# Kernel optimization log

Measured on AMD Instinct MI355X. Metric: run time of the kernel, lower is better.

The kernel has to match this reference:

```python
import jax, jax.numpy as jnp
import numpy as np

D = 1024       # d_model
H = 16         # n_heads
N = 8          # ortho_dim
NSKEW = N * (N - 1) // 2
MAX_ANGLE = 0.5
B, T = 4, 4096
IDX_I, IDX_J = np.triu_indices(N, k=1)


def setup_inputs() -> dict:
    key = jax.random.key(0)
    ks = jax.random.split(key, 8)
    s = 0.02
    w = lambda k, shape: jax.random.normal(k, shape, jnp.float32) * s
    return {
        "x": jax.random.normal(ks[0], (B, T, D), jnp.float32),
        "W_skew": w(ks[1], (D, H * NSKEW)),
        "W_k": w(ks[2], (D, H * N)),
        "W_v": w(ks[3], (D, H * N)),
        "W_q": w(ks[4], (D, H * N)),
        "W_beta": w(ks[5], (D, H)),
        "b_beta": w(ks[6], (H,)),
        "W_o": w(ks[7], (H * N, D)),
    }


def _forward(x, W_skew, W_k, W_v, W_q, W_beta, b_beta, W_o):
    Bb, Tt, _ = x.shape
    # skew-symmetric generator -> rotation O_t = expm(skew)
    skew_flat = MAX_ANGLE * jnp.tanh(x @ W_skew).reshape(Bb, Tt, H, NSKEW)
    skew = jnp.zeros((Bb, Tt, H, N, N), x.dtype)
    skew = skew.at[..., IDX_I, IDX_J].set(skew_flat)
    skew = skew.at[..., IDX_J, IDX_I].set(-skew_flat)
    O = jax.vmap(jax.scipy.linalg.expm)(skew.reshape(-1, N, N)).reshape(Bb, Tt, H, N, N)

    k = (x @ W_k).reshape(Bb, Tt, H, N)
    k = k / jnp.maximum(jnp.linalg.norm(k, axis=-1, keepdims=True), 1e-6)
    v = (x @ W_v).reshape(Bb, Tt, H, N)
    q = (x @ W_q).reshape(Bb, Tt, H, N)
    beta = jax.nn.sigmoid(x @ W_beta + b_beta)  # [B,T,H]

    def step(c, inp):
        O_t, k_t, v_t, b_t, q_t = inp  # [B,H,n,n], [B,H,n], ...
        # rotation conjugation: O c O^T
        c_rot = jnp.einsum('bhij,bhjk,bhlk->bhil', O_t, c, O_t)
        # rank-1 erase: c_rot - beta * k (k^T c_rot); rank-1 write: + beta * k v^T
        kc = jnp.einsum('bhi,bhij->bhj', k_t, c_rot)
        b = b_t[..., None, None]
        c_new = c_rot - b * k_t[..., None] * kc[..., None, :] + b * k_t[..., None] * v_t[..., None, :]
        o_t = jnp.einsum('bhi,bhij->bhj', q_t, c_new)  # readout q . c_t
        return c_new, o_t

    c0 = jnp.zeros((Bb, H, N, N), x.dtype)
    tfirst = lambda a: jnp.moveaxis(a, 1, 0)
    _, o = jax.lax.scan(step, c0, (tfirst(O), tfirst(k), tfirst(v), tfirst(beta), tfirst(q)))
    o = jnp.moveaxis(o, 0, 1).reshape(Bb, Tt, H * N)
    return o @ W_o


def reference(x, W_skew, W_k, W_v, W_q, W_beta, b_beta, W_o):
    return _forward(x, W_skew, W_k, W_v, W_q, W_beta, b_beta, W_o)
```

## Files before the change

kernel.cpp:

```cpp
#include <hip/hip_runtime.h>

typedef unsigned short u16;
typedef unsigned int u32;
typedef __attribute__((ext_vector_type(4))) float f32x4;
typedef __attribute__((ext_vector_type(8))) short short8;
typedef __attribute__((ext_vector_type(4))) unsigned int u32x4;

#define DEV __device__ __forceinline__

DEV float bf2f(u16 u){ union{u32 i; float f;} x; x.i = ((u32)u)<<16; return x.f; }
DEV u16 f2bf(float f){ union{u32 i; float f;} x; x.f = f; u32 r = x.i + 0x7fffu + ((x.i>>16)&1u); return (u16)(r>>16); }

union U8 { u16 u[8]; short8 s; };

DEV void gl16(const u16* g, u16* l){
  __builtin_amdgcn_global_load_lds(
      (const __attribute__((address_space(1))) u32*)g,
      (__attribute__((address_space(3))) u32*)l, 16, 0, 0);
}

DEV float fast_htanh(float v){
  float vc = fminf(fmaxf(v, -15.f), 15.f);
  float e = __expf(2.f*vc);
  return 0.5f*(e - 1.f)*__builtin_amdgcn_rcpf(e + 1.f);
}
DEV float fast_sigmoid(float v){
  float e = __expf(-v);
  return __builtin_amdgcn_rcpf(1.f + e);
}

__global__ __launch_bounds__(256) void splitx_kernel(const float* __restrict__ x,
    u16* __restrict__ xh, u16* __restrict__ xl)
{
  size_t base = ((size_t)blockIdx.x*256 + threadIdx.x) * 8;
  f32x4 a = *(const f32x4*)(x + base), b = *(const f32x4*)(x + base + 4);
  U8 h, l;
  #pragma unroll
  for (int e=0;e<4;e++){
    u16 hh = f2bf(a[e]); h.u[e]   = hh; l.u[e]   = f2bf(a[e] - bf2f(hh));
    u16 gg = f2bf(b[e]); h.u[4+e] = gg; l.u[4+e] = f2bf(b[e] - bf2f(gg));
  }
  *(short8*)(xh + base) = h.s;
  *(short8*)(xl + base) = l.s;
}

__global__ __launch_bounds__(256) void concat_kernel(
    const float* __restrict__ Wskew, const float* __restrict__ Wk, const float* __restrict__ Wv,
    const float* __restrict__ Wq, const float* __restrict__ Wbeta, const float* __restrict__ Wo,
    u16* __restrict__ Wh, u16* __restrict__ Wl, u16* __restrict__ WoT)
{
  int idx = blockIdx.x*256 + threadIdx.x;
  if (idx < 896*1024){
    int n = idx >> 10, kk = idx & 1023;
    float v;
    if (n < 448)      v = Wskew[kk*448 + n];
    else if (n < 576) v = Wk[kk*128 + (n-448)];
    else if (n < 704) v = Wv[kk*128 + (n-576)];
    else if (n < 832) v = Wq[kk*128 + (n-704)];
    else if (n < 848) v = Wbeta[kk*16 + (n-832)];
    else              v = 0.f;
    u16 h = f2bf(v);
    Wh[idx] = h;
    Wl[idx] = f2bf(v - bf2f(h));
  } else {
    int r = idx - 896*1024;
    int n = r >> 7, kk = r & 127;
    WoT[r] = f2bf(Wo[kk*1024 + n]);
  }
}

__global__ __launch_bounds__(256) void gemm_proj_kernel(
    const u16* __restrict__ Ah, const u16* __restrict__ Al,
    const u16* __restrict__ Bh, const u16* __restrict__ Bl,
    float* __restrict__ C, const float* __restrict__ bias)
{
  __shared__ u16 L[2*4*4096];
  const int tid = threadIdx.x;
  const int wave = tid >> 6;
  const int lane = tid & 63;
  const int quad = lane >> 4, l15 = lane & 15;
  const int m0 = blockIdx.x * 128, n0 = blockIdx.y * 128;
  const bool full = (blockIdx.y < 4);
  const int wm = (wave >> 1) * 64, wn = (wave & 1) * 64;
  const bool wantLow = full && !(blockIdx.y == 3 && wn == 64);
  const bool skipBl1 = (blockIdx.y == 3);
  const int K = 1024, ldc = 896;
  const int sr = tid >> 2;
  const int sc = tid & 3;
  const int fS = (sr & 3) ^ ((sr >> 2) & 3);
  const int scS = ((sc ^ fS) << 3);
  const size_t gA0 = (size_t)(m0 + sr)*K + scS, gA1 = gA0 + (size_t)64*K;
  const size_t gB0 = (size_t)(n0 + sr)*K + scS, gB1 = gB0 + (size_t)64*K;
  const int d0 = tid*8, d1 = d0 + 2048;
  const int fR = (l15 & 3) ^ ((l15 >> 2) & 3);
  const int rq = ((quad ^ fR) << 3);

  auto STAGE = [&](int buf, int kb){
    u16* Lb = L + buf*16384;
    gl16(Ah + gA0 + kb, Lb + d0);
    gl16(Ah + gA1 + kb, Lb + d1);
    gl16(Bh + gB0 + kb, Lb + 4096 + d0);
    gl16(Bh + gB1 + kb, Lb + 4096 + d1);
    if (full){
      gl16(Al + gA0 + kb, Lb + 8192 + d0);
      gl16(Al + gA1 + kb, Lb + 8192 + d1);
      gl16(Bl + gB0 + kb, Lb + 12288 + d0);
      if (!skipBl1) gl16(Bl + gB1 + kb, Lb + 12288 + d1);
    }
  };

  f32x4 acc[4][4] = {};
  STAGE(0, 0);
  __syncthreads();
  int cur = 0;
  for (int kb = 0; kb < K; kb += 32){
    if (kb + 32 < K) STAGE(cur^1, kb + 32);
    u16* Lb = L + cur*16384;
    short8 afh[4], bfh[4];
    #pragma unroll
    for (int mi=0;mi<4;mi++) afh[mi] = *(const short8*)&Lb[(wm + mi*16 + l15)*32 + rq];
    #pragma unroll
    for (int ni=0;ni<4;ni++) bfh[ni] = *(const short8*)&Lb[4096 + (wn + ni*16 + l15)*32 + rq];
    #pragma unroll
    for (int mi=0;mi<4;mi++)
      #pragma unroll
      for (int ni=0;ni<4;ni++)
        acc[mi][ni] = __builtin_amdgcn_mfma_f32_16x16x32_bf16(afh[mi], bfh[ni], acc[mi][ni], 0,0,0);
    if (wantLow){
      short8 afl[4], bfl[4];
      #pragma unroll
      for (int mi=0;mi<4;mi++) afl[mi] = *(const short8*)&Lb[8192 + (wm + mi*16 + l15)*32 + rq];
      #pragma unroll
      for (int ni=0;ni<4;ni++) bfl[ni] = *(const short8*)&Lb[12288 + (wn + ni*16 + l15)*32 + rq];
      #pragma unroll
      for (int mi=0;mi<4;mi++)
        #pragma unroll
        for (int ni=0;ni<4;ni++){
          acc[mi][ni] = __builtin_amdgcn_mfma_f32_16x16x32_bf16(afh[mi], bfl[ni], acc[mi][ni], 0,0,0);
          acc[mi][ni] = __builtin_amdgcn_mfma_f32_16x16x32_bf16(afl[mi], bfh[ni], acc[mi][ni], 0,0,0);
        }
    }
    __syncthreads();
    cur ^= 1;
  }
  #pragma unroll
  for (int mi=0;mi<4;mi++){
    #pragma unroll
    for (int ni=0;ni<4;ni++){
      const int col = n0 + wn + ni*16 + l15;
      const int rb_ = m0 + wm + mi*16 + quad*4;
      #pragma unroll
      for (int r=0;r<4;r++){
        float v = acc[mi][ni][r];
        const int row = rb_ + r;
        if (col < 448) v = fast_htanh(v);
        else if (col >= 832 && col < 848) v = fast_sigmoid(v + bias[col-832]);
        C[(size_t)row*ldc + col] = v;
      }
    }
  }
}

__global__ __launch_bounds__(256) void gemm_out_kernel(
    const u16* __restrict__ A, const u16* __restrict__ Bt, float* __restrict__ C)
{
  __shared__ u16 L[2*2*4096];
  const int tid = threadIdx.x;
  const int wave = tid >> 6;
  const int lane = tid & 63;
  const int quad = lane >> 4, l15 = lane & 15;
  const int m0 = blockIdx.x * 128, n0 = blockIdx.y * 128;
  const int wm = (wave >> 1) * 64, wn = (wave & 1) * 64;
  const int K = 128, ldc = 1024;
  const int sr = tid >> 2;
  const int sc = tid & 3;
  const int fS = (sr & 3) ^ ((sr >> 2) & 3);
  const int scS = ((sc ^ fS) << 3);
  const size_t gA0 = (size_t)(m0 + sr)*K + scS, gA1 = gA0 + (size_t)64*K;
  const size_t gB0 = (size_t)(n0 + sr)*K + scS, gB1 = gB0 + (size_t)64*K;
  const int d0 = tid*8, d1 = d0 + 2048;
  const int fR = (l15 & 3) ^ ((l15 >> 2) & 3);
  const int rq = ((quad ^ fR) << 3);

  auto STAGE = [&](int buf, int kb){
    u16* Lb = L + buf*8192;
    gl16(A  + gA0 + kb, Lb + d0);
    gl16(A  + gA1 + kb, Lb + d1);
    gl16(Bt + gB0 + kb, Lb + 4096 + d0);
    gl16(Bt + gB1 + kb, Lb + 4096 + d1);
  };

  f32x4 acc[4][4] = {};
  STAGE(0, 0);
  __syncthreads();
  int cur = 0;
  for (int kb = 0; kb < K; kb += 32){
    if (kb + 32 < K) STAGE(cur^1, kb + 32);
    u16* Lb = L + cur*8192;
    short8 af[4], bf8[4];
    #pragma unroll
    for (int mi=0;mi<4;mi++) af[mi] = *(const short8*)&Lb[(wm + mi*16 + l15)*32 + rq];
    #pragma unroll
    for (int ni=0;ni<4;ni++) bf8[ni] = *(const short8*)&Lb[4096 + (wn + ni*16 + l15)*32 + rq];
    #pragma unroll
    for (int mi=0;mi<4;mi++)
      #pragma unroll
      for (int ni=0;ni<4;ni++)
        acc[mi][ni] = __builtin_amdgcn_mfma_f32_16x16x32_bf16(af[mi], bf8[ni], acc[mi][ni], 0,0,0);
    __syncthreads();
    cur ^= 1;
  }
  #pragma unroll
  for (int mi=0;mi<4;mi++)
    #pragma unroll
    for (int ni=0;ni<4;ni++){
      const int col = n0 + wn + ni*16 + l15;
      const int rb_ = m0 + wm + mi*16 + quad*4;
      #pragma unroll
      for (int r=0;r<4;r++)
        C[(size_t)(rb_ + r)*ldc + col] = acc[mi][ni][r];
    }
}

__device__ constexpr int TRI_I[28] = {0,0,0,0,0,0,0, 1,1,1,1,1,1, 2,2,2,2,2, 3,3,3,3, 4,4,4, 5,5, 6};
__device__ constexpr int TRI_J[28] = {1,2,3,4,5,6,7, 2,3,4,5,6,7, 3,4,5,6,7, 4,5,6,7, 5,6,7, 6,7, 7};

__global__ __launch_bounds__(64) __attribute__((amdgpu_waves_per_eu(1, 2)))
void expm_scan_kernel(const float* __restrict__ proj, u16* __restrict__ ORbf, float* __restrict__ Pfin)
{
  __shared__ float S0[16*64*4];
  const int t = threadIdx.x;
  const int s = blockIdx.x >> 6, c = blockIdx.x & 63;
  const int b = s >> 4, h = s & 15;
  const int row = b*4096 + c*64 + t;
  const float* sk = proj + (size_t)row*896 + h*28;

  float v[28];
  {
    f32x4 vv[7];
    #pragma unroll
    for (int i=0;i<7;i++) vv[i] = *(const f32x4*)(sk + 4*i);
    #pragma unroll
    for (int i=0;i<28;i++) v[i] = vv[i>>2][i&3] * 0.0625f;
  }

  float M[64], T[64];
  #pragma unroll
  for (int i=0;i<8;i++){
    #pragma unroll
    for (int jj=0;jj<8;jj++){
      float bv = 0.f;
      if (i < jj){ const int k = i*7 - (i*(i-1))/2 + jj - i - 1; bv =  v[k]; }
      if (i > jj){ const int k = jj*7 - (jj*(jj-1))/2 + i - jj - 1; bv = -v[k]; }
      M[i*8+jj] = bv*(1.f/6.f) + ((i==jj)?1.f:0.f);
    }
  }
  const float coef[5] = {0.2f, 0.25f, 1.f/3.f, 0.5f, 1.f};
  #pragma unroll
  for (int st=0; st<5; st++){
    #pragma unroll
    for (int i=0;i<8;i++){
      float rowv[8];
      #pragma unroll
      for (int a=0;a<8;a++) rowv[a] = M[i*8+a];
      #pragma unroll
      for (int cc=0;cc<8;cc++){
        float acc = 0.f;
        #pragma unroll
        for (int a=0;a<8;a++){
          if (a == cc) continue;
          const int k = (a<cc) ? (a*7 - (a*(a-1))/2 + cc - a - 1)
                               : (cc*7 - (cc*(cc-1))/2 + a - cc - 1);
          if (a<cc) acc = fmaf( rowv[a], v[k], acc);
          else      acc = fmaf(-rowv[a], v[k], acc);
        }
        M[i*8+cc] = acc*coef[st] + ((i==cc)?1.f:0.f);
      }
    }
  }
  #pragma unroll
  for (int sq=0; sq<4; sq++){
    #pragma unroll
    for (int i=0;i<8;i++)
      #pragma unroll
      for (int cc=0;cc<8;cc++){
        float acc = 0.f;
        #pragma unroll
        for (int a=0;a<8;a++) acc = fmaf(M[i*8+a], M[a*8+cc], acc);
        T[i*8+cc] = acc;
      }
    #pragma unroll
    for (int f=0;f<64;f++) M[f] = T[f];
  }
  #pragma unroll
  for (int j=0;j<16;j++){
    f32x4 w = {M[4*j], M[4*j+1], M[4*j+2], M[4*j+3]};
    *(f32x4*)&S0[(j*64 + t)*4] = w;
  }
  __syncthreads();

  #pragma unroll
  for (int d=0; d<6; d++){
    const int off = 1 << d;
    if (t >= off){
      float Q[64];
      #pragma unroll
      for (int j=0;j<16;j++){
        f32x4 x = *(const f32x4*)&S0[(j*64 + (t-off))*4];
        Q[4*j]=x[0]; Q[4*j+1]=x[1]; Q[4*j+2]=x[2]; Q[4*j+3]=x[3];
      }
      #pragma unroll
      for (int i=0;i<8;i++){
        float r[8];
        #pragma unroll
        for (int cc=0;cc<8;cc++){
          float acc = 0.f;
          #pragma unroll
          for (int a=0;a<8;a++) acc = fmaf(M[i*8+a], Q[a*8+cc], acc);
          r[cc] = acc;
        }
        #pragma unroll
        for (int cc=0;cc<8;cc++) M[i*8+cc] = r[cc];
      }
    }
    if (d < 5){
      #pragma unroll
      for (int j=0;j<16;j++){
        f32x4 w = {M[4*j], M[4*j+1], M[4*j+2], M[4*j+3]};
        *(f32x4*)&S0[(j*64 + t)*4] = w;
      }
      __syncthreads();
    }
  }

  u16* dst = ORbf + ((size_t)s*4096 + (size_t)c*64 + t)*64;
  #pragma unroll
  for (int g=0; g<8; g++){
    u32 p0 = (u32)f2bf(M[0*8+g]) | ((u32)f2bf(M[1*8+g])<<16);
    u32 p1 = (u32)f2bf(M[2*8+g]) | ((u32)f2bf(M[3*8+g])<<16);
    u32 p2 = (u32)f2bf(M[4*8+g]) | ((u32)f2bf(M[5*8+g])<<16);
    u32 p3 = (u32)f2bf(M[6*8+g]) | ((u32)f2bf(M[7*8+g])<<16);
    u32x4 pk = {p0,p1,p2,p3};
    *(u32x4*)(void*)(dst + g*8) = pk;
  }
  if (t == 63){
    float* pf = Pfin + ((size_t)s*64 + c)*64;
    #pragma unroll
    for (int a=0;a<8;a++){
      f32x4 w  = {M[0*8+a], M[1*8+a], M[2*8+a], M[3*8+a]};
      f32x4 w2 = {M[4*8+a], M[5*8+a], M[6*8+a], M[7*8+a]};
      *(f32x4*)(pf + a*8)     = w;
      *(f32x4*)(pf + a*8 + 4) = w2;
    }
  }
}

DEV void load16(const float* p, f32x4* M){
  #pragma unroll
  for (int q=0;q<16;q++) M[q] = *(const f32x4*)(p + 4*q);
}
DEV void load16bf(const u16* p, f32x4* M){
  #pragma unroll
  for (int q=0;q<8;q++){
    u32x4 x = *(const u32x4*)(const void*)(p + q*8);
    f32x4 a = { bf2f((u16)x[0]), bf2f((u16)(x[0]>>16)), bf2f((u16)x[1]), bf2f((u16)(x[1]>>16)) };
    f32x4 b = { bf2f((u16)x[2]), bf2f((u16)(x[2]>>16)), bf2f((u16)x[3]), bf2f((u16)(x[3]>>16)) };
    M[2*q] = a; M[2*q+1] = b;
  }
}
DEV void rm_matvec8(const f32x4* M16, const float* x, float* res){
  #pragma unroll
  for (int i=0;i<8;i++){
    float acc = 0.f;
    #pragma unroll
    for (int a=0;a<8;a++) acc = fmaf(M16[2*i + (a>>2)][a&3], x[a], acc);
    res[i] = acc;
  }
}
DEV void cm_matvec8(const f32x4* M16, const float* x, float* res){
  #pragma unroll
  for (int i=0;i<8;i++){
    float acc = 0.f;
    #pragma unroll
    for (int a=0;a<8;a++) acc = fmaf(M16[2*a + (i>>2)][i&3], x[a], acc);
    res[i] = acc;
  }
}

__global__ __launch_bounds__(64) __attribute__((amdgpu_waves_per_eu(1, 2)))
void chunkscan_kernel(const float* __restrict__ Pfin, float* __restrict__ Rbase)
{
  __shared__ float S[64*68];
  const int t = threadIdx.x;
  const int s = blockIdx.x;
  float M[64];
  const float* qs = Pfin + ((size_t)s*64 + t)*64;
  #pragma unroll
  for (int j=0;j<16;j++){
    f32x4 x = *(const f32x4*)(qs + 4*j);
    M[4*j]=x[0]; M[4*j+1]=x[1]; M[4*j+2]=x[2]; M[4*j+3]=x[3];
  }
  #pragma unroll
  for (int j=0;j<16;j++){
    f32x4 w = {M[4*j],M[4*j+1],M[4*j+2],M[4*j+3]};
    *(f32x4*)&S[t*68 + 4*j] = w;
  }
  __syncthreads();
  #pragma unroll
  for (int d=0; d<6; d++){
    const int off = 1 << d;
    if (t >= off){
      float Q[64];
      const float* p = &S[(t-off)*68];
      #pragma unroll
      for (int j=0;j<16;j++){
        f32x4 x = *(const f32x4*)(p + 4*j);
        Q[4*j]=x[0]; Q[4*j+1]=x[1]; Q[4*j+2]=x[2]; Q[4*j+3]=x[3];
      }
      float R[64];
      #pragma unroll
      for (int cc=0;cc<8;cc++)
        #pragma unroll
        for (int i=0;i<8;i++){
          float acc = 0.f;
          #pragma unroll
          for (int a=0;a<8;a++) acc = fmaf(M[a*8+i], Q[cc*8+a], acc);
          R[cc*8+i] = acc;
        }
      #pragma unroll
      for (int f=0;f<64;f++) M[f] = R[f];
    }
    if (d < 5){
      #pragma unroll
      for (int j=0;j<16;j++){
        f32x4 w = {M[4*j],M[4*j+1],M[4*j+2],M[4*j+3]};
        *(f32x4*)&S[t*68 + 4*j] = w;
      }
      __syncthreads();
    }
  }
  if (t < 63){
    float* dst = Rbase + ((size_t)s*64 + t + 1)*64;
    #pragma unroll
    for (int j=0;j<16;j++){
      f32x4 w = {M[4*j],M[4*j+1],M[4*j+2],M[4*j+3]};
      *(f32x4*)(dst + 4*j) = w;
    }
  }
  if (t == 0){
    float* dst = Rbase + (size_t)s*64*64;
    #pragma unroll
    for (int cc=0;cc<8;cc++)
      #pragma unroll
      for (int i=0;i<8;i++) dst[cc*8+i] = (i==cc) ? 1.f : 0.f;
  }
}

__global__ __launch_bounds__(256) void rotate_kvq_kernel(const u16* __restrict__ ORbf, const float* __restrict__ Rbase,
    float* __restrict__ proj)
{
  int tid = blockIdx.x*256 + threadIdx.x;
  int s = tid >> 12, t = tid & 4095;
  int c = t >> 6;
  int b = s >> 4, h = s & 15;
  int row = b*4096 + t;
  const u16* slot = ORbf + ((size_t)s*4096 + t)*64;
  float* pr = proj + (size_t)row*896;
  float k[8], v[8], q[8];
  { f32x4 a = *(const f32x4*)(pr+448+h*8), b2 = *(const f32x4*)(pr+452+h*8);
    #pragma unroll
    for (int i=0;i<4;i++){ k[i]=a[i]; k[4+i]=b2[i]; } }
  { f32x4 a = *(const f32x4*)(pr+576+h*8), b2 = *(const f32x4*)(pr+580+h*8);
    #pragma unroll
    for (int i=0;i<4;i++){ v[i]=a[i]; v[4+i]=b2[i]; } }
  { f32x4 a = *(const f32x4*)(pr+704+h*8), b2 = *(const f32x4*)(pr+708+h*8);
    #pragma unroll
    for (int i=0;i<4;i++){ q[i]=a[i]; q[4+i]=b2[i]; } }
  float nn = 0.f;
  #pragma unroll
  for (int i=0;i<8;i++) nn = fmaf(k[i],k[i],nn);
  float inv = 1.f / fmaxf(sqrtf(nn), 1e-6f);
  #pragma unroll
  for (int i=0;i<8;i++) k[i] *= inv;

  f32x4 M[16];
  load16bf(slot, M);
  float uk[8], uv[8], uq[8];
  rm_matvec8(M, k, uk);
  rm_matvec8(M, v, uv);
  rm_matvec8(M, q, uq);
  load16(Rbase + ((size_t)s*64 + c)*64, M);
  float kt[8], vt[8], qt[8];
  rm_matvec8(M, uk, kt);
  rm_matvec8(M, uv, vt);
  rm_matvec8(M, uq, qt);

  float beta = pr[832+h];
  float qk = 0.f;
  #pragma unroll
  for (int j=0;j<8;j++) qk = fmaf(kt[j], qt[j], qk);
  float* sip = pr + h*28;
  f32x4 w0={kt[0],kt[1],kt[2],kt[3]}, w1={kt[4],kt[5],kt[6],kt[7]};
  f32x4 w2={vt[0],vt[1],vt[2],vt[3]}, w3={vt[4],vt[5],vt[6],vt[7]};
  f32x4 w4={qt[0],qt[1],qt[2],qt[3]}, w5={qt[4],qt[5],qt[6],qt[7]};
  f32x4 w6={beta, qk, 0.f, 0.f};
  *(f32x4*)(sip)=w0; *(f32x4*)(sip+4)=w1; *(f32x4*)(sip+8)=w2; *(f32x4*)(sip+12)=w3;
  *(f32x4*)(sip+16)=w4; *(f32x4*)(sip+20)=w5; *(f32x4*)(sip+24)=w6;
}

__global__ __launch_bounds__(256) void scan_pass1_kernel(const float* __restrict__ proj,
    float* __restrict__ Mbuf, float* __restrict__ wbuf)
{
  int tid = blockIdx.x*256 + threadIdx.x;
  int task = tid >> 3, j = tid & 7;
  int s = task >> 8, c = task & 255;
  int b = s >> 4, h = s & 15;
  const float* rec = proj + ((size_t)b*4096 + (size_t)c*16)*896 + h*28;
  float m[8], w[8];
  #pragma unroll
  for (int i=0;i<8;i++){ m[i] = (i==j)?1.f:0.f; w[i] = 0.f; }
  f32x4 k0 = *(const f32x4*)(rec), k1 = *(const f32x4*)(rec+4);
  float vt = rec[8+j];
  float beta = rec[24];
  for (int tt=0; tt<16; tt++){
    const float* pn = rec + (size_t)(tt+1)*896;
    f32x4 nk0 = *(const f32x4*)(pn), nk1 = *(const f32x4*)(pn+4);
    float nvt = pn[8+j];
    float nbeta = pn[24];
    float s1, s2;
    s1 = ((k0[0]*m[0] + k0[1]*m[1]) + (k0[2]*m[2] + k0[3]*m[3]))
       + ((k1[0]*m[4] + k1[1]*m[5]) + (k1[2]*m[6] + k1[3]*m[7]));
    s2 = ((k0[0]*w[0] + k0[1]*w[1]) + (k0[2]*w[2] + k0[3]*w[3]))
       + ((k1[0]*w[4] + k1[1]*w[5]) + (k1[2]*w[6] + k1[3]*w[7]));
    float c1 = -beta*s1, c2 = beta*(vt - s2);
    #pragma unroll
    for (int i=0;i<4;i++){ m[i] = fmaf(k0[i], c1, m[i]); m[4+i] = fmaf(k1[i], c1, m[4+i]); }
    #pragma unroll
    for (int i=0;i<4;i++){ w[i] = fmaf(k0[i], c2, w[i]); w[4+i] = fmaf(k1[i], c2, w[4+i]); }
    k0=nk0; k1=nk1; vt=nvt; beta=nbeta;
  }
  float* md = Mbuf + (size_t)task*64 + j*8;
  float* wd = wbuf + (size_t)task*64 + j*8;
  f32x4 m0={m[0],m[1],m[2],m[3]}, m1={m[4],m[5],m[6],m[7]};
  f32x4 w0={w[0],w[1],w[2],w[3]}, w1={w[4],w[5],w[6],w[7]};
  *(f32x4*)(md) = m0; *(f32x4*)(md+4) = m1;
  *(f32x4*)(wd) = w0; *(f32x4*)(wd+4) = w1;
}

__global__ __launch_bounds__(512) void scan_mid_kernel(const float* __restrict__ Mbuf,
    const float* __restrict__ wbuf, float* __restrict__ dstart)
{
  __shared__ float SM[256*68];
  __shared__ float SW[256*68];
  const int tid = threadIdx.x;
  const int c = tid >> 1, g = tid & 1;
  const int s = blockIdx.x;
  const size_t base = (size_t)s*256*64;
  const float* mp = Mbuf + base + (size_t)c*64 + 32*g;
  const float* wp = wbuf + base + (size_t)c*64 + 32*g;
  float W[32];
  {
    float* sm = &SM[c*68 + 32*g];
    float* sw = &SW[c*68 + 32*g];
    #pragma unroll
    for (int j=0;j<8;j++){
      f32x4 a = *(const f32x4*)(mp + 4*j);
      f32x4 b = *(const f32x4*)(wp + 4*j);
      *(f32x4*)(sm + 4*j) = a;
      *(f32x4*)(sw + 4*j) = b;
      W[4*j]=b[0]; W[4*j+1]=b[1]; W[4*j+2]=b[2]; W[4*j+3]=b[3];
    }
  }
  __syncthreads();
  for (int d=0; d<8; d++){
    const int off = 1 << d;
    const bool act = (c >= off);
    float Mo[64], pM[32], pW[32];
    if (act){
      const float* om = &SM[c*68];
      #pragma unroll
      for (int j=0;j<16;j++){
        f32x4 x = *(const f32x4*)(om + 4*j);
        Mo[4*j]=x[0]; Mo[4*j+1]=x[1]; Mo[4*j+2]=x[2]; Mo[4*j+3]=x[3];
      }
      const float* qm = &SM[(c-off)*68 + 32*g];
      const float* qw = &SW[(c-off)*68 + 32*g];
      #pragma unroll
      for (int j=0;j<8;j++){
        f32x4 x = *(const f32x4*)(qm + 4*j);
        f32x4 y = *(const f32x4*)(qw + 4*j);
        pM[4*j]=x[0]; pM[4*j+1]=x[1]; pM[4*j+2]=x[2]; pM[4*j+3]=x[3];
        pW[4*j]=y[0]; pW[4*j+1]=y[1]; pW[4*j+2]=y[2]; pW[4*j+3]=y[3];
      }
    }
    __syncthreads();
    if (act){
      float nM[32], nW[32];
      #pragma unroll
      for (int cl=0; cl<4; cl++){
        #pragma unroll
        for (int i=0;i<8;i++){
          float aM = 0.f, aW = 0.f;
          #pragma unroll
          for (int a=0;a<8;a++){
            aM = fmaf(Mo[a*8+i], pM[cl*8+a], aM);
            aW = fmaf(Mo[a*8+i], pW[cl*8+a], aW);
          }
          nM[cl*8+i] = aM;
          nW[cl*8+i] = aW + W[cl*8+i];
        }
      }
      float* sm = &SM[c*68 + 32*g];
      float* sw = &SW[c*68 + 32*g];
      #pragma unroll
      for (int j=0;j<8;j++){
        f32x4 x = {nM[4*j], nM[4*j+1], nM[4*j+2], nM[4*j+3]};
        f32x4 y = {nW[4*j], nW[4*j+1], nW[4*j+2], nW[4*j+3]};
        *(f32x4*)(sm + 4*j) = x;
        *(f32x4*)(sw + 4*j) = y;
      }
      #pragma unroll
      for (int f=0;f<32;f++) W[f] = nW[f];
    }
    __syncthreads();
  }
  if (c < 255){
    float* dd = dstart + base + (size_t)(c+1)*64 + 32*g;
    #pragma unroll
    for (int j=0;j<8;j++){
      f32x4 y = {W[4*j],W[4*j+1],W[4*j+2],W[4*j+3]};
      *(f32x4*)(dd + 4*j) = y;
    }
  }
  if (c == 0){
    float* dd = dstart + base + 32*g;
    f32x4 z = {0.f,0.f,0.f,0.f};
    #pragma unroll
    for (int j=0;j<8;j++) *(f32x4*)(dd + 4*j) = z;
  }
}

__global__ __launch_bounds__(256) void scan_pass2_kernel(const float* __restrict__ proj,
    const float* __restrict__ dstart, float* __restrict__ oo)
{
  int tid = blockIdx.x*256 + threadIdx.x;
  int task = tid >> 3, j = tid & 7;
  int s = task >> 8, c = task & 255;
  int b = s >> 4, h = s & 15;
  const float* rec = proj + ((size_t)b*4096 + (size_t)c*16)*896 + h*28;
  float* op = oo + (((size_t)s*4096 + (size_t)c*16)*8) + j;
  float d[8];
  { const float* ds = dstart + (size_t)task*64 + j*8;
    f32x4 a = *(const f32x4*)(ds), b2 = *(const f32x4*)(ds+4);
    #pragma unroll
    for (int i=0;i<4;i++){ d[i]=a[i]; d[4+i]=b2[i]; } }
  f32x4 k0 = *(const f32x4*)(rec),    k1 = *(const f32x4*)(rec+4);
  f32x4 q0 = *(const f32x4*)(rec+16), q1 = *(const f32x4*)(rec+20);
  f32x4 mb = *(const f32x4*)(rec+24);
  float vt = rec[8+j];
  for (int tt=0; tt<16; tt++){
    const float* pn = rec + (size_t)(tt+1)*896;
    f32x4 nk0 = *(const f32x4*)(pn),    nk1 = *(const f32x4*)(pn+4);
    f32x4 nq0 = *(const f32x4*)(pn+16), nq1 = *(const f32x4*)(pn+20);
    f32x4 nmb = *(const f32x4*)(pn+24);
    float nvt = pn[8+j];
    float kd, qd;
    kd = ((k0[0]*d[0] + k0[1]*d[1]) + (k0[2]*d[2] + k0[3]*d[3]))
       + ((k1[0]*d[4] + k1[1]*d[5]) + (k1[2]*d[6] + k1[3]*d[7]));
    qd = ((q0[0]*d[0] + q0[1]*d[1]) + (q0[2]*d[2] + q0[3]*d[3]))
       + ((q1[0]*d[4] + q1[1]*d[5]) + (q1[2]*d[6] + q1[3]*d[7]));
    float w_ = mb[0] * (vt - kd);
    #pragma unroll
    for (int i=0;i<4;i++){ d[i] = fmaf(k0[i], w_, d[i]); d[4+i] = fmaf(k1[i], w_, d[4+i]); }
    op[(size_t)tt*8] = fmaf(mb[1], w_, qd);
    k0=nk0; k1=nk1; q0=nq0; q1=nq1; mb=nmb; vt=nvt;
  }
}

__global__ __launch_bounds__(256) void rotout_kernel(const u16* __restrict__ ORbf, const float* __restrict__ Rbase,
                                                     const float* __restrict__ oo, u16* __restrict__ obf)
{
  int tid = blockIdx.x*256 + threadIdx.x;
  int s = tid >> 12, t = tid & 4095;
  int c = t >> 6;
  int b = s >> 4, h = s & 15;
  int row = b*4096 + t;
  float u[8];
  { const float* up = oo + ((size_t)s*4096 + t)*8;
    f32x4 a = *(const f32x4*)(up), b2 = *(const f32x4*)(up+4);
    #pragma unroll
    for (int i=0;i<4;i++){ u[i]=a[i]; u[4+i]=b2[i]; } }
  f32x4 M[16];
  load16(Rbase + ((size_t)s*64 + c)*64, M);
  float w[8];
  cm_matvec8(M, u, w);
  load16bf(ORbf + ((size_t)s*4096 + t)*64, M);
  float o[8];
  cm_matvec8(M, w, o);
  u32 p0 = (u32)f2bf(o[0]) | ((u32)f2bf(o[1])<<16);
  u32 p1 = (u32)f2bf(o[2]) | ((u32)f2bf(o[3])<<16);
  u32 p2 = (u32)f2bf(o[4]) | ((u32)f2bf(o[5])<<16);
  u32 p3 = (u32)f2bf(o[6]) | ((u32)f2bf(o[7])<<16);
  u32x4 pk = {p0,p1,p2,p3};
  *(u32x4*)(void*)(obf + (size_t)row*128 + h*8) = pk;
}

extern "C" void kernel_launch(void* const* d_in, const int* in_sizes, int n_in,
                              void* d_out, int out_size, void* d_ws, size_t ws_size,
                              hipStream_t stream)
{
  const float* x     = (const float*)d_in[0];
  const float* Wskew = (const float*)d_in[1];
  const float* Wk    = (const float*)d_in[2];
  const float* Wv    = (const float*)d_in[3];
  const float* Wq    = (const float*)d_in[4];
  const float* Wbeta = (const float*)d_in[5];
  const float* bbeta = (const float*)d_in[6];
  const float* Wo    = (const float*)d_in[7];

  char* w = (char*)d_ws; size_t off = 0;
  auto alloc = [&](size_t bytes)->void*{ void* p = w + off; off += (bytes + 255) & ~(size_t)255; return p; };
  u16*   Wh     = (u16*)  alloc((size_t)896*1024*2);
  u16*   Wl     = (u16*)  alloc((size_t)896*1024*2);
  u16*   WoT    = (u16*)  alloc((size_t)1024*128*2);
  float* proj   = (float*)alloc((size_t)16384*896*4);
  char*  ORal   = (char*) alloc((size_t)64*1024*1024);
  float* Pfin   = (float*)alloc((size_t)4096*64*4);
  float* Rbase  = (float*)alloc((size_t)64*64*64*4);
  float* oo     = (float*)alloc((size_t)262144*8*4);
  float* Mbuf   = (float*)alloc((size_t)16384*64*4);
  float* wbuf   = (float*)alloc((size_t)16384*64*4);
  float* dstart = (float*)alloc((size_t)16384*64*4);
  u16*   ORbf   = (u16*)ORal;
  u16*   xh     = (u16*)ORal;
  u16*   xl     = xh + (size_t)16384*1024;
  u16*   obf    = (u16*)proj;

  hipLaunchKernelGGL(splitx_kernel, dim3(8192), dim3(256), 0, stream, x, xh, xl);
  hipLaunchKernelGGL(concat_kernel, dim3(4096), dim3(256), 0, stream,
                     Wskew, Wk, Wv, Wq, Wbeta, Wo, Wh, Wl, WoT);
  hipLaunchKernelGGL(gemm_proj_kernel, dim3(128,7), dim3(256), 0, stream,
                     xh, xl, Wh, Wl, proj, bbeta);
  hipLaunchKernelGGL(expm_scan_kernel, dim3(4096), dim3(64), 0, stream, proj, ORbf, Pfin);
  hipLaunchKernelGGL(chunkscan_kernel, dim3(64), dim3(64), 0, stream, Pfin, Rbase);
  hipLaunchKernelGGL(rotate_kvq_kernel, dim3(1024), dim3(256), 0, stream, ORbf, Rbase, proj);
  hipLaunchKernelGGL(scan_pass1_kernel, dim3(512), dim3(256), 0, stream, proj, Mbuf, wbuf);
  hipLaunchKernelGGL(scan_mid_kernel, dim3(64), dim3(512), 0, stream, Mbuf, wbuf, dstart);
  hipLaunchKernelGGL(scan_pass2_kernel, dim3(512), dim3(256), 0, stream, proj, dstart, oo);
  hipLaunchKernelGGL(rotout_kernel, dim3(1024), dim3(256), 0, stream, ORbf, Rbase, oo, obf);
  hipLaunchKernelGGL(gemm_out_kernel, dim3(128,8), dim3(256), 0, stream,
                     obf, WoT, (float*)d_out);
}
```

Before: 360.2 us.

## Halve scan chunk length and pair chunks in mid-scan to double parallelism

The chunked linear scan now uses 512 chunks of 8 timesteps per sequence instead of 256 chunks of 16, so pass1 and pass2 launch twice as many threads, each with half the serial loop. The mid kernel first composes adjacent chunk pairs in registers so it still runs a 256-element Hillis-Steele scan. It then expands the odd-chunk start states from the previous pair prefix. This shortens the serial dependency chains in pass1 and pass2, at the cost of larger intermediate buffers and extra matrix work and global traffic in the mid kernel.

```diff
diff --git a/kernel.cpp b/kernel.cpp
--- a/kernel.cpp
+++ b/kernel.cpp
@@ -513,16 +513,16 @@
 {
   int tid = blockIdx.x*256 + threadIdx.x;
   int task = tid >> 3, j = tid & 7;
-  int s = task >> 8, c = task & 255;
+  int s = task >> 9, c = task & 511;
   int b = s >> 4, h = s & 15;
-  const float* rec = proj + ((size_t)b*4096 + (size_t)c*16)*896 + h*28;
+  const float* rec = proj + ((size_t)b*4096 + (size_t)c*8)*896 + h*28;
   float m[8], w[8];
   #pragma unroll
   for (int i=0;i<8;i++){ m[i] = (i==j)?1.f:0.f; w[i] = 0.f; }
   f32x4 k0 = *(const f32x4*)(rec), k1 = *(const f32x4*)(rec+4);
   float vt = rec[8+j];
   float beta = rec[24];
-  for (int tt=0; tt<16; tt++){
+  for (int tt=0; tt<8; tt++){
     const float* pn = rec + (size_t)(tt+1)*896;
     f32x4 nk0 = *(const f32x4*)(pn), nk1 = *(const f32x4*)(pn+4);
     float nvt = pn[8+j];
@@ -553,38 +553,66 @@
   __shared__ float SM[256*68];
   __shared__ float SW[256*68];
   const int tid = threadIdx.x;
-  const int c = tid >> 1, g = tid & 1;
+  const int p = tid >> 1, g = tid & 1;
   const int s = blockIdx.x;
-  const size_t base = (size_t)s*256*64;
-  const float* mp = Mbuf + base + (size_t)c*64 + 32*g;
-  const float* wp = wbuf + base + (size_t)c*64 + 32*g;
-  float W[32];
-  {
-    float* sm = &SM[c*68 + 32*g];
-    float* sw = &SW[c*68 + 32*g];
-    #pragma unroll
-    for (int j=0;j<8;j++){
-      f32x4 a = *(const f32x4*)(mp + 4*j);
-      f32x4 b = *(const f32x4*)(wp + 4*j);
-      *(f32x4*)(sm + 4*j) = a;
-      *(f32x4*)(sw + 4*j) = b;
-      W[4*j]=b[0]; W[4*j+1]=b[1]; W[4*j+2]=b[2]; W[4*j+3]=b[3];
-    }
-  }
+  const size_t base = (size_t)s*512*64;
+  float M1[64];
+  { const float* m1p = Mbuf + base + (size_t)(2*p+1)*64;
+    #pragma unroll
+    for (int j=0;j<16;j++){
+      f32x4 x = *(const f32x4*)(m1p + 4*j);
+      M1[4*j]=x[0]; M1[4*j+1]=x[1]; M1[4*j+2]=x[2]; M1[4*j+3]=x[3];
+    } }
+  float A[32], R[32], W[32];
+  { const float* m0p = Mbuf + base + (size_t)(2*p)*64 + 32*g;
+    #pragma unroll
+    for (int j=0;j<8;j++){ f32x4 x = *(const f32x4*)(m0p + 4*j); A[4*j]=x[0]; A[4*j+1]=x[1]; A[4*j+2]=x[2]; A[4*j+3]=x[3]; } }
+  #pragma unroll
+  for (int cl=0; cl<4; cl++)
+    #pragma unroll
+    for (int i=0;i<8;i++){
+      float acc = 0.f;
+      #pragma unroll
+      for (int a=0;a<8;a++) acc = fmaf(M1[a*8+i], A[cl*8+a], acc);
+      R[cl*8+i] = acc;
+    }
+  { float* sm = &SM[p*68 + 32*g];
+    #pragma unroll
+    for (int j=0;j<8;j++){ f32x4 x = {R[4*j],R[4*j+1],R[4*j+2],R[4*j+3]}; *(f32x4*)(sm + 4*j) = x; } }
+  { const float* w0p = wbuf + base + (size_t)(2*p)*64 + 32*g;
+    #pragma unroll
+    for (int j=0;j<8;j++){ f32x4 x = *(const f32x4*)(w0p + 4*j); A[4*j]=x[0]; A[4*j+1]=x[1]; A[4*j+2]=x[2]; A[4*j+3]=x[3]; } }
+  #pragma unroll
+  for (int cl=0; cl<4; cl++)
+    #pragma unroll
+    for (int i=0;i<8;i++){
+      float acc = 0.f;
+      #pragma unroll
+      for (int a=0;a<8;a++) acc = fmaf(M1[a*8+i], A[cl*8+a], acc);
+      R[cl*8+i] = acc;
+    }
+  { const float* w1p = wbuf + base + (size_t)(2*p+1)*64 + 32*g;
+    #pragma unroll
+    for (int j=0;j<8;j++){ f32x4 x = *(const f32x4*)(w1p + 4*j); R[4*j]+=x[0]; R[4*j+1]+=x[1]; R[4*j+2]+=x[2]; R[4*j+3]+=x[3]; } }
+  { float* sw = &SW[p*68 + 32*g];
+    #pragma unroll
+    for (int j=0;j<8;j++){ f32x4 x = {R[4*j],R[4*j+1],R[4*j+2],R[4*j+3]}; *(f32x4*)(sw + 4*j) = x; } }
+  #pragma unroll
+  for (int f=0;f<32;f++) W[f] = R[f];
   __syncthreads();
   for (int d=0; d<8; d++){
     const int off = 1 << d;
-    const bool act = (c >= off);
+    const bool act = (p >= off);
     float Mo[64], pM[32], pW[32];
     if (act){
-      const float* om = &SM[c*68];
+      const float* om = &SM[p*68];
       #pragma unroll
       for (int j=0;j<16;j++){
         f32x4 x = *(const f32x4*)(om + 4*j);
         Mo[4*j]=x[0]; Mo[4*j+1]=x[1]; Mo[4*j+2]=x[2]; Mo[4*j+3]=x[3];
       }
-      const float* qm = &SM[(c-off)*68 + 32*g];
-      const float* qw = &SW[(c-off)*68 + 32*g];
+      const float* qm = &SM[(p-off)*68 + 32*g];
+      const float* qw = &SW[(p-off)*68 + 32*g];
       #pragma unroll
       for (int j=0;j<8;j++){
         f32x4 x = *(const f32x4*)(qm + 4*j);
@@ -610,8 +638,8 @@
           nW[cl*8+i] = aW + W[cl*8+i];
         }
       }
-      float* sm = &SM[c*68 + 32*g];
-      float* sw = &SW[c*68 + 32*g];
+      float* sm = &SM[p*68 + 32*g];
+      float* sw = &SW[p*68 + 32*g];
       #pragma unroll
       for (int j=0;j<8;j++){
         f32x4 x = {nM[4*j], nM[4*j+1], nM[4*j+2], nM[4*j+3]};
@@ -624,20 +652,52 @@
     }
     __syncthreads();
   }
-  if (c < 255){
-    float* dd = dstart + base + (size_t)(c+1)*64 + 32*g;
-    #pragma unroll
-    for (int j=0;j<8;j++){
-      f32x4 y = {W[4*j],W[4*j+1],W[4*j+2],W[4*j+3]};
-      *(f32x4*)(dd + 4*j) = y;
-    }
-  }
-  if (c == 0){
+  if (p < 255){
+    float* dd = dstart + base + (size_t)(2*p+2)*64 + 32*g;
+    #pragma unroll
+    for (int j=0;j<8;j++){ f32x4 y = {W[4*j],W[4*j+1],W[4*j+2],W[4*j+3]}; *(f32x4*)(dd + 4*j) = y; }
+  }
+  if (p == 0){
     float* dd = dstart + base + 32*g;
     f32x4 z = {0.f,0.f,0.f,0.f};
     #pragma unroll
     for (int j=0;j<8;j++) *(f32x4*)(dd + 4*j) = z;
   }
+  float Dp[32];
+  if (p == 0){
+    #pragma unroll
+    for (int f=0;f<32;f++) Dp[f] = 0.f;
+  } else {
+    const float* swp = &SW[(p-1)*68 + 32*g];
+    #pragma unroll
+    for (int j=0;j<8;j++){ f32x4 x = *(const f32x4*)(swp + 4*j); Dp[4*j]=x[0]; Dp[4*j+1]=x[1]; Dp[4*j+2]=x[2]; Dp[4*j+3]=x[3]; }
+  }
+  float M0[64];
+  { const float* m0p = Mbuf + base + (size_t)(2*p)*64;
+    #pragma unroll
+    for (int j=0;j<16;j++){
+      f32x4 x = *(const f32x4*)(m0p + 4*j);
+      M0[4*j]=x[0]; M0[4*j+1]=x[1]; M0[4*j+2]=x[2]; M0[4*j+3]=x[3];
+    } }
+  { const float* w0p = wbuf + base + (size_t)(2*p)*64 + 32*g;
+    float* dd = dstart + base + (size_t)(2*p+1)*64 + 32*g;
+    #pragma unroll
+    for (int cl=0; cl<4; cl++){
+      f32x4 wq0 = *(const f32x4*)(w0p + cl*8);
+      f32x4 wq1 = *(const f32x4*)(w0p + cl*8 + 4);
+      float r[8];
+      #pragma unroll
+      for (int i=0;i<8;i++){
+        float acc = 0.f;
+        #pragma unroll
+        for (int a=0;a<8;a++) acc = fmaf(M0[a*8+i], Dp[cl*8+a], acc);
+        r[i] = acc;
+      }
+      f32x4 y0 = {r[0]+wq0[0], r[1]+wq0[1], r[2]+wq0[2], r[3]+wq0[3]};
+      f32x4 y1 = {r[4]+wq1[0], r[5]+wq1[1], r[6]+wq1[2], r[7]+wq1[3]};
+      *(f32x4*)(dd + cl*8)     = y0;
+      *(f32x4*)(dd + cl*8 + 4) = y1;
+    } }
 }
 
 __global__ __launch_bounds__(256) void scan_pass2_kernel(const float* __restrict__ proj,
@@ -645,10 +705,10 @@
 {
   int tid = blockIdx.x*256 + threadIdx.x;
   int task = tid >> 3, j = tid & 7;
-  int s = task >> 8, c = task & 255;
+  int s = task >> 9, c = task & 511;
   int b = s >> 4, h = s & 15;
-  const float* rec = proj + ((size_t)b*4096 + (size_t)c*16)*896 + h*28;
-  float* op = oo + (((size_t)s*4096 + (size_t)c*16)*8) + j;
+  const float* rec = proj + ((size_t)b*4096 + (size_t)c*8)*896 + h*28;
+  float* op = oo + (((size_t)s*4096 + (size_t)c*8)*8) + j;
   float d[8];
   { const float* ds = dstart + (size_t)task*64 + j*8;
     f32x4 a = *(const f32x4*)(ds), b2 = *(const f32x4*)(ds+4);
@@ -658,7 +718,7 @@
   f32x4 q0 = *(const f32x4*)(rec+16), q1 = *(const f32x4*)(rec+20);
   f32x4 mb = *(const f32x4*)(rec+24);
   float vt = rec[8+j];
-  for (int tt=0; tt<16; tt++){
+  for (int tt=0; tt<8; tt++){
     const float* pn = rec + (size_t)(tt+1)*896;
     f32x4 nk0 = *(const f32x4*)(pn),    nk1 = *(const f32x4*)(pn+4);
     f32x4 nq0 = *(const f32x4*)(pn+16), nq1 = *(const f32x4*)(pn+20);
@@ -728,9 +788,9 @@
   float* Pfin   = (float*)alloc((size_t)4096*64*4);
   float* Rbase  = (float*)alloc((size_t)64*64*64*4);
   float* oo     = (float*)alloc((size_t)262144*8*4);
-  float* Mbuf   = (float*)alloc((size_t)16384*64*4);
-  float* wbuf   = (float*)alloc((size_t)16384*64*4);
-  float* dstart = (float*)alloc((size_t)16384*64*4);
+  float* Mbuf   = (float*)alloc((size_t)32768*64*4);
+  float* wbuf   = (float*)alloc((size_t)32768*64*4);
+  float* dstart = (float*)alloc((size_t)32768*64*4);
   u16*   ORbf   = (u16*)ORal;
   u16*   xh     = (u16*)ORal;
   u16*   xl     = xh + (size_t)16384*1024;
@@ -744,9 +804,9 @@
   hipLaunchKernelGGL(expm_scan_kernel, dim3(4096), dim3(64), 0, stream, proj, ORbf, Pfin);
   hipLaunchKernelGGL(chunkscan_kernel, dim3(64), dim3(64), 0, stream, Pfin, Rbase);
   hipLaunchKernelGGL(rotate_kvq_kernel, dim3(1024), dim3(256), 0, stream, ORbf, Rbase, proj);
-  hipLaunchKernelGGL(scan_pass1_kernel, dim3(512), dim3(256), 0, stream, proj, Mbuf, wbuf);
+  hipLaunchKernelGGL(scan_pass1_kernel, dim3(1024), dim3(256), 0, stream, proj, Mbuf, wbuf);
   hipLaunchKernelGGL(scan_mid_kernel, dim3(64), dim3(512), 0, stream, Mbuf, wbuf, dstart);
-  hipLaunchKernelGGL(scan_pass2_kernel, dim3(512), dim3(256), 0, stream, proj, dstart, oo);
+  hipLaunchKernelGGL(scan_pass2_kernel, dim3(1024), dim3(256), 0, stream, proj, dstart, oo);
   hipLaunchKernelGGL(rotout_kernel, dim3(1024), dim3(256), 0, stream, ORbf, Rbase, oo, obf);
   hipLaunchKernelGGL(gemm_out_kernel, dim3(128,8), dim3(256), 0, stream,
                      obf, WoT, (float*)d_out);
```

Result: no change. 366.9 us (+1.9%).
